# Kernel optimization log

Measured on AMD Instinct MI355X. Metric: run time of the kernel, lower is better.

The kernel has to match this reference:

```python
import jax, jax.numpy as jnp
import numpy as np

N_QUBITS = 16
N_LAYERS = 4
N_ACTIONS = 6
BATCH = 512


def _apply_1q(state, U, wire):
    """Apply a single-qubit gate U to `wire` of batched state [B,2,...,2].
    U is [2,2] (shared) or [B,2,2] (per-sample)."""
    s = jnp.moveaxis(state, wire + 1, -1)
    if U.ndim == 2:
        s = jnp.einsum('ij,b...j->b...i', U, s)
    else:
        s = jnp.einsum('bij,b...j->b...i', U, s)
    return jnp.moveaxis(s, -1, wire + 1)


def _ry(theta):
    # RY(theta); theta scalar or [B]
    c = jnp.cos(theta / 2).astype(jnp.complex64)
    s = jnp.sin(theta / 2).astype(jnp.complex64)
    return jnp.stack([jnp.stack([c, -s], -1), jnp.stack([s, c], -1)], -2)


def _rot(phi, theta, omega):
    # PennyLane Rot = RZ(omega) RY(theta) RZ(phi)
    c = jnp.cos(theta / 2)
    s = jnp.sin(theta / 2)
    ep = jnp.exp(-0.5j * (phi + omega).astype(jnp.complex64))
    em = jnp.exp(-0.5j * (phi - omega).astype(jnp.complex64))
    m00 = ep * c
    m01 = -jnp.conj(em) * s
    m10 = em * s
    m11 = jnp.conj(ep) * c
    return jnp.stack([jnp.stack([m00, m01], -1), jnp.stack([m10, m11], -1)], -2)


def _cz_factor(wire):
    # diagonal CZ phase on wires (wire, wire+1): diag(1,1,1,-1)
    f = jnp.array([1, 1, 1, -1], dtype=jnp.complex64).reshape(2, 2)
    shape = (1,) + (1,) * wire + (2, 2) + (1,) * (N_QUBITS - wire - 2)
    return f.reshape(shape)


def _circuit(x, weights):
    # x: [B, n_qubits] angles; weights: [L, n_qubits, 3]
    B = x.shape[0]
    state = jnp.zeros((B,) + (2,) * N_QUBITS, dtype=jnp.complex64)
    state = state.at[(slice(None),) + (0,) * N_QUBITS].set(1.0)
    # AngleEmbedding: RY(x_i) on wire i (per-sample angles)
    for i in range(N_QUBITS):
        state = _apply_1q(state, _ry(x[:, i]), i)
    for l in range(N_LAYERS):
        for i in range(N_QUBITS):
            state = _apply_1q(state, _rot(weights[l, i, 0], weights[l, i, 1], weights[l, i, 2]), i)
        for i in range(N_QUBITS - 1):
            state = state * _cz_factor(i)
    probs = state.real ** 2 + state.imag ** 2  # [B,2,...,2]
    zs = []
    all_axes = tuple(range(1, N_QUBITS + 1))
    for i in range(N_QUBITS):
        pi = jnp.sum(probs, axis=tuple(a for a in all_axes if a != i + 1))  # [B,2]
        zs.append(pi[:, 0] - pi[:, 1])
    return jnp.stack(zs, axis=-1)  # [B, n_qubits] expval <Z_i>


def setup_inputs() -> dict:
    key = jax.random.key(0)
    k1, k2, k3, k4 = jax.random.split(key, 4)
    x = jax.random.uniform(k1, (BATCH, N_QUBITS), dtype=jnp.float32) * np.float32(np.pi)
    weights = jax.random.normal(k2, (N_LAYERS, N_QUBITS, 3), dtype=jnp.float32)
    fc_w = jax.random.normal(k3, (N_ACTIONS, N_QUBITS), dtype=jnp.float32) / np.float32(np.sqrt(N_QUBITS))
    fc_b = jax.random.normal(k4, (N_ACTIONS,), dtype=jnp.float32) * 0.01
    return {"x": x, "weights": weights, "fc_w": fc_w, "fc_b": fc_b}


def reference(x, weights, fc_w, fc_b):
    z = _circuit(x, weights).astype(jnp.float32)  # [B, n_qubits]
    return z @ fc_w.T + fc_b  # [B, n_actions]
```

## Files before the change

### kernel.cpp

```cpp
#include <hip/hip_runtime.h>

#define NQ 16
#define NL 4
#define NA 6
#define BATCH 512

#define A1_OFF 1024

__global__ __launch_bounds__(256)
void prep_kernel(const float* __restrict__ x,
                 const float* __restrict__ wt,
                 const float* __restrict__ fb,
                 float4* __restrict__ ws,
                 float* __restrict__ out)
{
    const int tid = threadIdx.x, blk = blockIdx.x;
    if (blk < 32) {
        const int t = blk * 256 + tid;
        const int b = t >> 4, w = t & 15;
        const float phi = wt[w * 3 + 0], th = wt[w * 3 + 1];
        float sp, cp, st, ct, sx, cx;
        sincosf(0.5f * phi, &sp, &cp);
        sincosf(0.5f * th,  &st, &ct);
        sincosf(0.5f * x[b * NQ + w], &sx, &cx);
        const float w00r =  ct * cp, w00i = -ct * sp;
        const float w01r = -st * cp, w01i = -st * sp;
        const float w10r =  st * cp, w10i = -st * sp;
        const float w11r =  ct * cp, w11i =  ct * sp;
        const float a00r =  w00r * cx + w01r * sx, a00i =  w00i * cx + w01i * sx;
        const float a01r = -w00r * sx + w01r * cx, a01i = -w00i * sx + w01i * cx;
        const float a10r =  w10r * cx + w11r * sx, a10i =  w10i * cx + w11i * sx;
        const float a11r = -w10r * sx + w11r * cx, a11i = -w10i * sx + w11i * cx;
        ws[A1_OFF + t * 2 + 0] = make_float4(a00r, a00i, a01r, a01i);
        ws[A1_OFF + t * 2 + 1] = make_float4(a11r, a11i, a10r, a10i);
    } else if (blk == 32) {
        if (tid < 48) {
            const int g = tid >> 4, w = tid & 15;
            const int l = g + 1;
            const float al = wt[((l - 1) * NQ + w) * 3 + 2] + wt[(l * NQ + w) * 3 + 0];
            const float th = wt[(l * NQ + w) * 3 + 1];
            float sa, ca, st, ct;
            sincosf(0.5f * al, &sa, &ca);
            sincosf(0.5f * th, &st, &ct);
            ws[tid * 2 + 0] = make_float4(ct * ca, -ct * sa, -st * ca, -st * sa);
            ws[tid * 2 + 1] = make_float4(ct * ca,  ct * sa,  st * ca, -st * sa);
        }
    } else {
        const int t = (blk - 33) * 256 + tid;
        if (t < BATCH * NA) out[t] = fb[t - (t / NA) * NA];
    }
}


__global__ __launch_bounds__(256, 8)
void qmain_kernel(const float4* __restrict__ ws,
                  const float* __restrict__ fw,
                  float* __restrict__ out)
{
    __shared__ float4 lm[4][NQ][2];
    __shared__ float zsh[4];

    const int tid = threadIdx.x;
    const int b   = blockIdx.x >> 2;

    if (tid < 128) {
        const int g = tid >> 5;
        ((float4*)lm)[tid] = (g == 0) ? ws[A1_OFF + (b << 5) + tid]
                                      : ws[tid - 32];
    }
    __syncthreads();

    const int lane = tid & 63;
    const int wv   = tid >> 6;
    const int qi   = ((blockIdx.x & 3) << 2) | wv;

    float ar0 = (lane == 0) ? 1.0f : 0.0f, ai0 = 0.0f;
    float ar1 = 0.0f, ai1 = 0.0f;

    const int n0 = lane << 1, n1 = n0 | 1;
    const float czs0 = (__popc((n0 & (n0 >> 1)) & 0x3F) & 1) ? -1.0f : 1.0f;
    const float czs1 = (__popc((n1 & (n1 >> 1)) & 0x3F) & 1) ? -1.0f : 1.0f;

#define GATE(J, G) do {                                                        \
    const int w_ = qi + (J) - 3;                                               \
    if (0 <= w_ && w_ < NQ) {                                                  \
        if ((J) == 0) {                                                        \
            const float4 r0 = lm[G][w_][0], r1 = lm[G][w_][1];                 \
            const float nr0 = r0.x*ar0 - r0.y*ai0 + r0.z*ar1 - r0.w*ai1;       \
            const float ni0 = r0.x*ai0 + r0.y*ar0 + r0.z*ai1 + r0.w*ar1;       \
            const float nr1 = r1.z*ar0 - r1.w*ai0 + r1.x*ar1 - r1.y*ai1;       \
            const float ni1 = r1.z*ai0 + r1.w*ar0 + r1.x*ai1 + r1.y*ar1;       \
            ar0 = nr0; ai0 = ni0; ar1 = nr1; ai1 = ni1;                        \
        } else {                                                               \
            const int m_   = 1 << ((J) - 1);                                   \
            const int row_ = (lane >> ((J) - 1)) & 1;                          \
            const float4 c = lm[G][w_][row_];                                  \
            const float pr0 = __shfl_xor(ar0, m_, 64);                         \
            const float pi0 = __shfl_xor(ai0, m_, 64);                         \
            const float pr1 = __shfl_xor(ar1, m_, 64);                         \
            const float pi1 = __shfl_xor(ai1, m_, 64);                         \
            const float t0r = c.x*ar0 - c.y*ai0 + c.z*pr0 - c.w*pi0;           \
            const float t0i = c.x*ai0 + c.y*ar0 + c.z*pi0 + c.w*pr0;           \
            const float t1r = c.x*ar1 - c.y*ai1 + c.z*pr1 - c.w*pi1;           \
            const float t1i = c.x*ai1 + c.y*ar1 + c.z*pi1 + c.w*pr1;           \
            ar0 = t0r; ai0 = t0i; ar1 = t1r; ai1 = t1i;                        \
        }                                                                      \
    }                                                                          \
} while (0)

#define CZ() do { ar0 *= czs0; ai0 *= czs0; ar1 *= czs1; ai1 *= czs1; } while (0)

    GATE(0,0); GATE(1,0); GATE(2,0); GATE(3,0); GATE(4,0); GATE(5,0); GATE(6,0);
    CZ();
    GATE(1,1); GATE(2,1); GATE(3,1); GATE(4,1); GATE(5,1);
    CZ();
    GATE(2,2); GATE(3,2); GATE(4,2);
    CZ();
    GATE(3,3);

#undef GATE
#undef CZ

    const float sm = ((lane >> 2) & 1) ? -1.0f : 1.0f;
    float p = sm * (ar0*ar0 + ai0*ai0 + ar1*ar1 + ai1*ai1);
#pragma unroll
    for (int off = 32; off > 0; off >>= 1)
        p += __shfl_xor(p, off, 64);

    if (lane == 0) zsh[wv] = p;
    __syncthreads();

    if (tid < NA) {
        const int q0 = (blockIdx.x & 3) << 2;
        const float* fwr = fw + tid * NQ + q0;
        const float acc = zsh[0]*fwr[0] + zsh[1]*fwr[1] + zsh[2]*fwr[2] + zsh[3]*fwr[3];
        atomicAdd(&out[b * NA + tid], acc);
    }
}

extern "C" void kernel_launch(void* const* d_in, const int* in_sizes, int n_in,
                              void* d_out, int out_size, void* d_ws, size_t ws_size,
                              hipStream_t stream) {
    const float* x    = (const float*)d_in[0];
    const float* wts  = (const float*)d_in[1];
    const float* fc_w = (const float*)d_in[2];
    const float* fc_b = (const float*)d_in[3];
    float* out  = (float*)d_out;
    float4* ws4 = (float4*)d_ws;

    prep_kernel<<<45, 256, 0, stream>>>(x, wts, fc_b, ws4, out);
    qmain_kernel<<<2048, 256, 0, stream>>>(ws4, fc_w, out);
}
```

Before: 68.84 us.

## Fuse prep and main kernels into one 1024-thread block per sample

Merges the gate-precompute kernel into the main kernel, so each block computes its own sample's gate matrices into shared memory. Each block now has 16 waves covering all 16 qubits, so the final linear layer is computed in-block and written directly instead of through atomics onto a bias-initialised output. This removes one kernel launch, the workspace round trip and the atomics. In exchange every block redoes the shared layer-gate trig, and the larger blocks may change occupancy.

```diff
diff --git a/kernel.cpp b/kernel.cpp
--- a/kernel.cpp
+++ b/kernel.cpp
@@ -5,74 +5,54 @@
 #define NA 6
 #define BATCH 512
 
-#define A1_OFF 1024
 
-__global__ __launch_bounds__(256)
-void prep_kernel(const float* __restrict__ x,
-                 const float* __restrict__ wt,
-                 const float* __restrict__ fb,
-                 float4* __restrict__ ws,
-                 float* __restrict__ out)
+__global__ __launch_bounds__(1024, 8)
+void qdqn_one_kernel(const float* __restrict__ x,
+                     const float* __restrict__ wt,
+                     const float* __restrict__ fw,
+                     const float* __restrict__ fb,
+                     float* __restrict__ out)
 {
-    const int tid = threadIdx.x, blk = blockIdx.x;
-    if (blk < 32) {
-        const int t = blk * 256 + tid;
-        const int b = t >> 4, w = t & 15;
-        const float phi = wt[w * 3 + 0], th = wt[w * 3 + 1];
-        float sp, cp, st, ct, sx, cx;
-        sincosf(0.5f * phi, &sp, &cp);
-        sincosf(0.5f * th,  &st, &ct);
-        sincosf(0.5f * x[b * NQ + w], &sx, &cx);
-        const float w00r =  ct * cp, w00i = -ct * sp;
-        const float w01r = -st * cp, w01i = -st * sp;
-        const float w10r =  st * cp, w10i = -st * sp;
-        const float w11r =  ct * cp, w11i =  ct * sp;
-        const float a00r =  w00r * cx + w01r * sx, a00i =  w00i * cx + w01i * sx;
-        const float a01r = -w00r * sx + w01r * cx, a01i = -w00i * sx + w01i * cx;
-        const float a10r =  w10r * cx + w11r * sx, a10i =  w10i * cx + w11i * sx;
-        const float a11r = -w10r * sx + w11r * cx, a11i = -w10i * sx + w11i * cx;
-        ws[A1_OFF + t * 2 + 0] = make_float4(a00r, a00i, a01r, a01i);
-        ws[A1_OFF + t * 2 + 1] = make_float4(a11r, a11i, a10r, a10i);
-    } else if (blk == 32) {
-        if (tid < 48) {
-            const int g = tid >> 4, w = tid & 15;
-            const int l = g + 1;
-            const float al = wt[((l - 1) * NQ + w) * 3 + 2] + wt[(l * NQ + w) * 3 + 0];
-            const float th = wt[(l * NQ + w) * 3 + 1];
+    __shared__ float4 lm[4][NQ][2];
+    __shared__ float zsh[NQ];
+
+    const int tid = threadIdx.x;
+    const int b   = blockIdx.x;
+
+    if (tid < 64) {
+        const int w = tid & 15;
+        const int g = tid >> 4;
+        float4 R0, R1;
+        if (g == 0) {
+            const float phi = wt[w * 3 + 0], th = wt[w * 3 + 1];
+            float sp, cp, st, ct, sx, cx;
+            sincosf(0.5f * phi, &sp, &cp);
+            sincosf(0.5f * th,  &st, &ct);
+            sincosf(0.5f * x[b * NQ + w], &sx, &cx);
+            const float w00r =  ct * cp, w00i = -ct * sp;
+            const float w01r = -st * cp, w01i = -st * sp;
+            const float w10r =  st * cp, w10i = -st * sp;
+            const float w11r =  ct * cp, w11i =  ct * sp;
+            R0 = make_float4( w00r*cx + w01r*sx,  w00i*cx + w01i*sx,
+                             -w00r*sx + w01r*cx, -w00i*sx + w01i*cx);
+            R1 = make_float4(-w10r*sx + w11r*cx, -w10i*sx + w11i*cx,
+                              w10r*cx + w11r*sx,  w10i*cx + w11i*sx);
+        } else {
+            const float al = wt[((g - 1) * NQ + w) * 3 + 2] + wt[(g * NQ + w) * 3 + 0];
+            const float th = wt[(g * NQ + w) * 3 + 1];
             float sa, ca, st, ct;
             sincosf(0.5f * al, &sa, &ca);
             sincosf(0.5f * th, &st, &ct);
-            ws[tid * 2 + 0] = make_float4(ct * ca, -ct * sa, -st * ca, -st * sa);
-            ws[tid * 2 + 1] = make_float4(ct * ca,  ct * sa,  st * ca, -st * sa);
+            R0 = make_float4(ct * ca, -ct * sa, -st * ca, -st * sa);
+            R1 = make_float4(ct * ca,  ct * sa,  st * ca, -st * sa);
         }
-    } else {
-        const int t = (blk - 33) * 256 + tid;
-        if (t < BATCH * NA) out[t] = fb[t - (t / NA) * NA];
-    }
-}
-
-
-__global__ __launch_bounds__(256, 8)
-void qmain_kernel(const float4* __restrict__ ws,
-                  const float* __restrict__ fw,
-                  float* __restrict__ out)
-{
-    __shared__ float4 lm[4][NQ][2];
-    __shared__ float zsh[4];
-
-    const int tid = threadIdx.x;
-    const int b   = blockIdx.x >> 2;
-
-    if (tid < 128) {
-        const int g = tid >> 5;
-        ((float4*)lm)[tid] = (g == 0) ? ws[A1_OFF + (b << 5) + tid]
-                                      : ws[tid - 32];
+        lm[g][w][0] = R0;
+        lm[g][w][1] = R1;
     }
     __syncthreads();
 
     const int lane = tid & 63;
-    const int wv   = tid >> 6;
-    const int qi   = ((blockIdx.x & 3) << 2) | wv;
+    const int qi   = tid >> 6;
 
     float ar0 = (lane == 0) ? 1.0f : 0.0f, ai0 = 0.0f;
     float ar1 = 0.0f, ai1 = 0.0f;
@@ -83,7 +63,7 @@
 
 #define GATE(J, G) do {                                                        \
     const int w_ = qi + (J) - 3;                                               \
-    if (0 <= w_ && w_ < NQ) {                                                  \
+    if (0 <= w_ && w_ < NQ) {                                \
         if ((J) == 0) {                                                        \
             const float4 r0 = lm[G][w_][0], r1 = lm[G][w_][1];                 \
             const float nr0 = r0.x*ar0 - r0.y*ai0 + r0.z*ar1 - r0.w*ai1;       \
@@ -126,15 +106,15 @@
 #pragma unroll
     for (int off = 32; off > 0; off >>= 1)
         p += __shfl_xor(p, off, 64);
-
-    if (lane == 0) zsh[wv] = p;
+    if (lane == 0) zsh[qi] = p;
     __syncthreads();
 
     if (tid < NA) {
-        const int q0 = (blockIdx.x & 3) << 2;
-        const float* fwr = fw + tid * NQ + q0;
-        const float acc = zsh[0]*fwr[0] + zsh[1]*fwr[1] + zsh[2]*fwr[2] + zsh[3]*fwr[3];
-        atomicAdd(&out[b * NA + tid], acc);
+        float acc = fb[tid];
+#pragma unroll
+        for (int i = 0; i < NQ; ++i)
+            acc += zsh[i] * fw[tid * NQ + i];
+        out[b * NA + tid] = acc;
     }
 }
 
@@ -145,9 +125,7 @@
     const float* wts  = (const float*)d_in[1];
     const float* fc_w = (const float*)d_in[2];
     const float* fc_b = (const float*)d_in[3];
-    float* out  = (float*)d_out;
-    float4* ws4 = (float4*)d_ws;
+    float* out = (float*)d_out;
 
-    prep_kernel<<<45, 256, 0, stream>>>(x, wts, fc_b, ws4, out);
-    qmain_kernel<<<2048, 256, 0, stream>>>(ws4, fc_w, out);
+    qdqn_one_kernel<<<BATCH, 1024, 0, stream>>>(x, wts, fc_w, fc_b, out);
 }
```

Result: faster. 66.50 us (-3.4%).
